# Kernel optimization log

Measured on AMD Instinct MI355X. Metric: run time of the kernel, lower is better.

Reference implementation:

```python
import jax, jax.numpy as jnp
import numpy as np

N_ROUTES = 7      # len(ROUTES): 3 unimodal + 3 bimodal + 1 trimodal routes
PC_DIM = 512      # primary capsule pose dim
MC_DIM = 128      # output (decision) capsule pose dim
K = 25            # num_classes (phenotypes)
NUM_ROUTING = 3   # routing iterations
B = 4096


def _layer_norm(x, gamma, beta, eps=1e-5):
    mu = jnp.mean(x, axis=-1, keepdims=True)
    var = jnp.var(x, axis=-1, keepdims=True)
    return (x - mu) * jax.lax.rsqrt(var + eps) * gamma + beta


def setup_inputs() -> dict:
    key = jax.random.key(0)
    ks = jax.random.split(key, 4)
    w_std = float(np.sqrt(K / (PC_DIM * N_ROUTES)))  # CapsuleFC weight init scale
    return {
        "prim_pose": jax.random.normal(ks[0], (B, N_ROUTES, PC_DIM), dtype=jnp.float32),
        "prim_act": jax.random.uniform(ks[1], (B, N_ROUTES), dtype=jnp.float32),
        "w": w_std * jax.random.normal(ks[2], (N_ROUTES, PC_DIM, K, MC_DIM), dtype=jnp.float32),
        "ln_gamma": jnp.ones((MC_DIM,), dtype=jnp.float32),
        "ln_beta": jnp.zeros((MC_DIM,), dtype=jnp.float32),
        "embedding": 0.02 * jax.random.normal(ks[3], (K, MC_DIM), dtype=jnp.float32),
        "bias": jnp.zeros((K,), dtype=jnp.float32),
    }


def reference(prim_pose, prim_act, w, ln_gamma, ln_beta, embedding, bias):
    # prim_pose: [B, N, D_in]; prim_act: [B, N]
    act = prim_act[..., None]                      # [B, N, 1]
    scale = 1.0 / np.sqrt(MC_DIM)
    # Votes are constant across routing iterations; hoist out of the loop.
    vote = jnp.einsum('bnd,ndmv->bnmv', prim_pose, w)  # [B, N, K, Dv]
    next_pose = None
    routing_coef = None
    for it in range(NUM_ROUTING):
        if next_pose is None:
            # iteration 0: uniform routing coefficients (softmax of zeros over out capsules)
            routing_coef = jnp.full((prim_pose.shape[0], N_ROUTES, K), 1.0 / K,
                                    dtype=prim_pose.dtype)
        else:
            # inverted dot-product attention: agreement between votes and current decision pose
            agree = jnp.einsum('bnmv,bmv->bnm', vote, next_pose) * scale
            routing_coef = jax.nn.softmax(agree, axis=-1)
        c = routing_coef * act                     # weight routing by primary activations
        next_pose = _layer_norm(jnp.einsum('bnm,bnmv->bmv', c, vote), ln_gamma, ln_beta)
        # act_type='ONES' -> decision activations are all ones (no effect on routing)
    logits = jnp.einsum('bmd,md->bm', next_pose, embedding) + bias  # [B, K]
    return logits, prim_act, routing_coef
```

## Files before the change

kernel.cpp:

```cpp
#include <hip/hip_runtime.h>
#include <hip/hip_bf16.h>
#include <math.h>

#define N_ROUTES 7
#define PC_DIM   512
#define MC_DIM   128
#define KCLS     25
#define BATCH    4096

#define ROW_IN   (N_ROUTES * PC_DIM)
#define JDIM     (KCLS * MC_DIM)
#define VOTE_B   (N_ROUTES * JDIM)

typedef __attribute__((ext_vector_type(8))) _Float16 half8;
typedef __attribute__((ext_vector_type(4))) float f32x4;

__device__ inline ushort f2h(float f) {
    _Float16 h = (_Float16)f;
    return __builtin_bit_cast(ushort, h);
}

__device__ inline float2 h2f2(uint u) {
    union { uint x; _Float16 h[2]; } c; c.x = u;
    return make_float2((float)c.h[0], (float)c.h[1]);
}

__device__ inline void load_lds16(const void* g, void* l) {
    __builtin_amdgcn_global_load_lds(
        (const __attribute__((address_space(1))) void*)g,
        (__attribute__((address_space(3))) void*)l, 16, 0, 0);
}

__global__ __launch_bounds__(256) void conv_pose(const float* __restrict__ p,
                                                 ushort* __restrict__ pb, int n8) {
    int i = blockIdx.x * 256 + threadIdx.x;
    if (i >= n8) return;
    const float4* s = (const float4*)p + (size_t)i * 2;
    float4 a = s[0], b = s[1];
    ushort t[8];
    t[0]=f2h(a.x); t[1]=f2h(a.y); t[2]=f2h(a.z); t[3]=f2h(a.w);
    t[4]=f2h(b.x); t[5]=f2h(b.y); t[6]=f2h(b.z); t[7]=f2h(b.w);
    *(uint4*)(pb + (size_t)i * 8) = *(uint4*)t;
}

__global__ __launch_bounds__(256) void conv_w(const float* __restrict__ w,
                                              ushort* __restrict__ wt) {
    __shared__ float t[32][65];
    const int j0 = blockIdx.x * 32, d0 = blockIdx.y * 64, r = blockIdx.z;
    const int jc = threadIdx.x & 31, dr0 = threadIdx.x >> 5;
    const float* wp = w + (size_t)r * PC_DIM * JDIM;
#pragma unroll
    for (int i = 0; i < 8; i++)
        t[jc][dr0 + i * 8] = wp[(size_t)(d0 + dr0 + i * 8) * JDIM + j0 + jc];
    __syncthreads();
    const int jr = threadIdx.x >> 3, dc = (threadIdx.x & 7) * 8;
    ushort o[8];
#pragma unroll
    for (int k = 0; k < 8; k++) o[k] = f2h(t[jr][dc + k]);
    ushort* op = wt + (size_t)r * JDIM * PC_DIM;
    *(uint4*)(op + (size_t)(j0 + jr) * PC_DIM + d0 + dc) = *(uint4*)o;
}


#define BAR() do { __builtin_amdgcn_sched_barrier(0); \
                   __builtin_amdgcn_s_barrier(); \
                   __builtin_amdgcn_sched_barrier(0); } while (0)
#define WAIT_LGKM0() do { asm volatile("s_waitcnt lgkmcnt(0)" ::: "memory"); \
                          __builtin_amdgcn_sched_barrier(0); } while (0)
#define WAIT_VM(n) do { asm volatile("s_waitcnt vmcnt(" #n ")" ::: "memory"); } while (0)

__global__ __launch_bounds__(256, 3) void vote_gemm_mfma(
        const ushort* __restrict__ poseb,
        const ushort* __restrict__ wt,
        ushort* __restrict__ vote,
        int rows) {
    __shared__ __align__(16) char smem[49152];

    int route, rowTile, jTile;
    {
        const int blk = blockIdx.x;
        if (gridDim.x == 5600) {
            const int x = blk & 7;
            const int g = blk >> 3;
            const int q = g / 25;
            jTile = g - q * 25;
            const int p = x * 28 + q;
            route = p >> 5;
            rowTile = p & 31;
        } else {
            rowTile = blk / 175;
            const int rem = blk - rowTile * 175;
            route = rem / 25;
            jTile = rem - route * 25;
        }
    }
    const int b0 = rowTile * 128;
    const int j0 = jTile * 128;

    const int tid = threadIdx.x;
    const int l = tid & 63, w = tid >> 6;
    const int wm = w >> 1, wn = w & 1;
    const int lm = l & 15, q4 = l >> 4;
    const int xr = (l >> 1) & 3;

    const ushort* Aptr = poseb + (size_t)route * PC_DIM;
    const ushort* Bptr = wt + (size_t)route * JDIM * PC_DIM;

    uint aof0, aof1, bof0, bof1;
    {
        int f, row, c, qg, ga;
        f = tid;        row = f >> 2; c = f & 3; qg = c ^ ((row >> 1) & 3);
        ga = b0 + row; if (ga >= rows) ga = rows - 1;
        aof0 = (uint)ga * ROW_IN + qg * 8;
        bof0 = (uint)(j0 + row) * PC_DIM + qg * 8;
        f = tid + 256;  row = f >> 2; c = f & 3; qg = c ^ ((row >> 1) & 3);
        ga = b0 + row; if (ga >= rows) ga = rows - 1;
        aof1 = (uint)ga * ROW_IN + qg * 8;
        bof1 = (uint)(j0 + row) * PC_DIM + qg * 8;
    }

    const int aBase = ((wm * 64 + lm) * 4 + (q4 ^ xr)) * 16;
    const int bBase = 8192 + ((wn * 64 + lm) * 4 + (q4 ^ xr)) * 16;

    f32x4 acc[4][4] = {};

#define STAGE(kt) do { \
        char* d_ = smem + (((kt) % 3) * 16384); \
        load_lds16(Aptr + aof0 + (kt) * 32, d_ + (size_t)tid * 16); \
        load_lds16(Aptr + aof1 + (kt) * 32, d_ + (size_t)(tid + 256) * 16); \
        load_lds16(Bptr + bof0 + (kt) * 32, d_ + 8192 + (size_t)tid * 16); \
        load_lds16(Bptr + bof1 + (kt) * 32, d_ + 8192 + (size_t)(tid + 256) * 16); \
    } while (0)

    STAGE(0); STAGE(1);
    WAIT_VM(4);
    BAR();

    half8 af[4], bf[4];

#pragma unroll
    for (int t = 0; t < 16; ++t) {
        if (t < 14) STAGE(t + 2);
        const char* bp_ = smem + ((t % 3) * 16384);
#pragma unroll
        for (int nt = 0; nt < 4; nt++)
            bf[nt] = *(const half8*)(bp_ + bBase + nt * 1024);
#pragma unroll
        for (int mt = 0; mt < 4; mt++)
            af[mt] = *(const half8*)(bp_ + aBase + mt * 1024);
        WAIT_LGKM0();
        __builtin_amdgcn_s_setprio(1);
#pragma unroll
        for (int mt = 0; mt < 4; mt++)
#pragma unroll
            for (int nt = 0; nt < 4; nt++)
                acc[mt][nt] = __builtin_amdgcn_mfma_f32_16x16x32_f16(
                    af[mt], bf[nt], acc[mt][nt], 0, 0, 0);
        __builtin_amdgcn_s_setprio(0);
        if (t < 14)       WAIT_VM(4);
        else if (t == 14) WAIT_VM(0);
        BAR();
    }

    float* ep = (float*)smem + w * 1088;
    const int erow = l >> 2, ec0 = (l & 3) * 16;
#pragma unroll
    for (int mt = 0; mt < 4; mt++) {
#pragma unroll
        for (int nt = 0; nt < 4; nt++)
#pragma unroll
            for (int i = 0; i < 4; i++)
                ep[(q4 * 4 + i) * 68 + nt * 16 + lm] = acc[mt][nt][i];
        asm volatile("s_waitcnt lgkmcnt(0)" ::: "memory");
        const int grow = b0 + wm * 64 + mt * 16 + erow;
        if (grow < rows) {
            ushort t16[16];
#pragma unroll
            for (int t8 = 0; t8 < 4; t8++) {
                float4 v = *(float4*)&ep[erow * 68 + ec0 + t8 * 4];
                t16[t8*4+0]=f2h(v.x); t16[t8*4+1]=f2h(v.y);
                t16[t8*4+2]=f2h(v.z); t16[t8*4+3]=f2h(v.w);
            }
            ushort* dst = vote + (size_t)grow * VOTE_B + route * JDIM + j0 + wn * 64 + ec0;
            ((uint4*)dst)[0] = ((uint4*)t16)[0];
            ((uint4*)dst)[1] = ((uint4*)t16)[1];
        }
        asm volatile("s_waitcnt lgkmcnt(0)" ::: "memory");
    }
}

__global__ __launch_bounds__(448) void routing_kernel(
        const ushort* __restrict__ vote16,
        const float* __restrict__ act,
        const float* __restrict__ gamma,
        const float* __restrict__ beta,
        const float* __restrict__ emb,
        const float* __restrict__ bias,
        float* __restrict__ out_logits,
        float* __restrict__ out_act,
        float* __restrict__ out_coef) {
    const int b = blockIdx.x;
    __shared__ float coef_s[N_ROUTES * KCLS];
    __shared__ float act_s[8];

    const int tid = threadIdx.x, l = tid & 63, wv = tid >> 6;
    const int sub = l & 15, mg = l >> 4;
    const int m = wv + 7 * mg;
    const bool mv = (m < KCLS);

    if (tid < N_ROUTES) {
        float a = act[(size_t)b * N_ROUTES + tid];
        act_s[tid] = a;
        out_act[(size_t)b * N_ROUTES + tid] = a;
    }

    float vf[N_ROUTES][8];
    if (mv) {
        const uint4* vb = (const uint4*)(vote16 + (size_t)b * VOTE_B);
#pragma unroll
        for (int n = 0; n < N_ROUTES; n++) {
            uint4 q = vb[n * 400 + m * 16 + sub];
            float2 f0 = h2f2(q.x), f1 = h2f2(q.y), f2 = h2f2(q.z), f3 = h2f2(q.w);
            vf[n][0] = f0.x; vf[n][1] = f0.y; vf[n][2] = f1.x; vf[n][3] = f1.y;
            vf[n][4] = f2.x; vf[n][5] = f2.y; vf[n][6] = f3.x; vf[n][7] = f3.y;
        }
    } else {
#pragma unroll
        for (int n = 0; n < N_ROUTES; n++)
#pragma unroll
            for (int j = 0; j < 8; j++) vf[n][j] = 0.f;
    }
    const int mc = mv ? m : 24;

    float g[8], be[8];
    *(float4*)(g)      = *(const float4*)(gamma + 8 * sub);
    *(float4*)(g + 4)  = *(const float4*)(gamma + 8 * sub + 4);
    *(float4*)(be)     = *(const float4*)(beta  + 8 * sub);
    *(float4*)(be + 4) = *(const float4*)(beta  + 8 * sub + 4);
    __syncthreads();

    const float scale = 0.088388347648318447f;
    float pose[8];

    auto update = [&](bool first) {
        float r[8];
#pragma unroll
        for (int j = 0; j < 8; j++) r[j] = 0.f;
#pragma unroll
        for (int n = 0; n < N_ROUTES; n++) {
            float c = first ? (act_s[n] * 0.04f) : (coef_s[n * KCLS + mc] * act_s[n]);
#pragma unroll
            for (int j = 0; j < 8; j++) r[j] += c * vf[n][j];
        }
        float S = 0.f, Q = 0.f;
#pragma unroll
        for (int j = 0; j < 8; j++) { S += r[j]; Q += r[j] * r[j]; }
#pragma unroll
        for (int o = 8; o; o >>= 1) {
            S += __shfl_xor(S, o);
            Q += __shfl_xor(Q, o);
        }
        float mean = S * 0.0078125f;
        float var  = Q * 0.0078125f - mean * mean;
        float rs   = rsqrtf(var + 1e-5f);
#pragma unroll
        for (int j = 0; j < 8; j++) pose[j] = (r[j] - mean) * rs * g[j] + be[j];
    };

    update(true);
    __syncthreads();

    const int sgrp = tid >> 5, slane = tid & 31;

    for (int it = 1; it < 3; it++) {
        float d[N_ROUTES];
#pragma unroll
        for (int n = 0; n < N_ROUTES; n++) {
            float t = 0.f;
#pragma unroll
            for (int j = 0; j < 8; j++) t += vf[n][j] * pose[j];
            d[n] = t;
        }
#pragma unroll
        for (int o = 8; o; o >>= 1)
#pragma unroll
            for (int n = 0; n < N_ROUTES; n++) d[n] += __shfl_xor(d[n], o);
        if (sub == 0 && mv) {
#pragma unroll
            for (int n = 0; n < N_ROUTES; n++) coef_s[n * KCLS + m] = d[n] * scale;
        }
        __syncthreads();
        if (sgrp < N_ROUTES) {
            float c = (slane < KCLS) ? coef_s[sgrp * KCLS + slane] : -1e30f;
            float mx = c;
#pragma unroll
            for (int o = 16; o; o >>= 1) mx = fmaxf(mx, __shfl_xor(mx, o, 32));
            float e = (slane < KCLS) ? expf(c - mx) : 0.f;
            float s = e;
#pragma unroll
            for (int o = 16; o; o >>= 1) s += __shfl_xor(s, o, 32);
            if (slane < KCLS) coef_s[sgrp * KCLS + slane] = e / s;
        }
        __syncthreads();
        update(false);
        if (it == 1) __syncthreads();
    }

    float e[8];
    *(float4*)(e)     = *(const float4*)(emb + mc * MC_DIM + 8 * sub);
    *(float4*)(e + 4) = *(const float4*)(emb + mc * MC_DIM + 8 * sub + 4);
    float dd = 0.f;
#pragma unroll
    for (int j = 0; j < 8; j++) dd += pose[j] * e[j];
#pragma unroll
    for (int o = 8; o; o >>= 1) dd += __shfl_xor(dd, o);
    if (sub == 0 && mv) out_logits[(size_t)b * KCLS + m] = dd + bias[m];

    if (tid < N_ROUTES * KCLS)
        out_coef[(size_t)b * (N_ROUTES * KCLS) + tid] = coef_s[tid];
}

extern "C" void kernel_launch(void* const* d_in, const int* in_sizes, int n_in,
                              void* d_out, int out_size, void* d_ws, size_t ws_size,
                              hipStream_t stream) {
    const float* pose  = (const float*)d_in[0];
    const float* act   = (const float*)d_in[1];
    const float* w     = (const float*)d_in[2];
    const float* gamma = (const float*)d_in[3];
    const float* beta  = (const float*)d_in[4];
    const float* emb   = (const float*)d_in[5];
    const float* bias  = (const float*)d_in[6];

    float* out        = (float*)d_out;
    float* out_logits = out;
    float* out_act    = out + BATCH * KCLS;
    float* out_coef   = out + BATCH * KCLS + BATCH * N_ROUTES;

    const size_t wt_bytes    = (size_t)N_ROUTES * JDIM * PC_DIM * 2;
    const size_t poseb_bytes = (size_t)BATCH * ROW_IN * 2;
    ushort* wt    = (ushort*)d_ws;
    ushort* poseb = (ushort*)((char*)d_ws + wt_bytes);
    ushort* voteh = (ushort*)((char*)d_ws + wt_bytes + poseb_bytes);

    size_t rem = ws_size > wt_bytes + poseb_bytes ? ws_size - wt_bytes - poseb_bytes : 0;
    size_t cap = rem / ((size_t)VOTE_B * 2);
    int chunk;
    if (cap >= (size_t)BATCH)  chunk = BATCH;
    else if (cap >= 128)       chunk = (int)(cap & ~(size_t)127);
    else                       chunk = (int)(cap > 0 ? cap : 1);

    conv_w<<<dim3(JDIM / 32, PC_DIM / 64, N_ROUTES), 256, 0, stream>>>(w, wt);
    const int n8 = BATCH * ROW_IN / 8;
    conv_pose<<<(n8 + 255) / 256, 256, 0, stream>>>(pose, poseb, n8);

    for (int b0 = 0; b0 < BATCH; b0 += chunk) {
        int rows = BATCH - b0 < chunk ? BATCH - b0 : chunk;
        int nRowTiles = (rows + 127) / 128;
        vote_gemm_mfma<<<nRowTiles * 175, 256, 0, stream>>>(
            poseb + (size_t)b0 * ROW_IN, wt, voteh, rows);
        routing_kernel<<<rows, 448, 0, stream>>>(
            voteh,
            act + (size_t)b0 * N_ROUTES,
            gamma, beta, emb, bias,
            out_logits + (size_t)b0 * KCLS,
            out_act    + (size_t)b0 * N_ROUTES,
            out_coef   + (size_t)b0 * N_ROUTES * KCLS);
    }
}
```

Before: 335.5 us.

## Double-buffer LDS fragment reads in vote GEMM to overlap with MFMA

Restructures the vote GEMM main loop so fragments for the next k-tile are read from LDS into a second register set while MFMAs run on the current set. This removes the explicit lgkmcnt(0) wait before each MFMA block. The epilogue now alternates between two LDS staging regions so the trailing lgkmcnt wait can be dropped. The extra fragment registers raise register pressure, which may hurt occupancy at three blocks per CU.

```diff
diff --git a/kernel.cpp b/kernel.cpp
--- a/kernel.cpp
+++ b/kernel.cpp
@@ -65,8 +65,6 @@
 #define BAR() do { __builtin_amdgcn_sched_barrier(0); \
                    __builtin_amdgcn_s_barrier(); \
                    __builtin_amdgcn_sched_barrier(0); } while (0)
-#define WAIT_LGKM0() do { asm volatile("s_waitcnt lgkmcnt(0)" ::: "memory"); \
-                          __builtin_amdgcn_sched_barrier(0); } while (0)
 #define WAIT_VM(n) do { asm volatile("s_waitcnt vmcnt(" #n ")" ::: "memory"); } while (0)
 
 __global__ __launch_bounds__(256, 3) void vote_gemm_mfma(
@@ -132,40 +130,53 @@
         load_lds16(Bptr + bof1 + (kt) * 32, d_ + 8192 + (size_t)(tid + 256) * 16); \
     } while (0)
 
+#define READF(kt, AF, BF) do { \
+        const char* rp_ = smem + (((kt) % 3) * 16384); \
+        _Pragma("unroll") for (int i_ = 0; i_ < 4; i_++) { \
+            AF[i_] = *(const half8*)(rp_ + aBase + i_ * 1024); \
+            BF[i_] = *(const half8*)(rp_ + bBase + i_ * 1024); \
+        } \
+    } while (0)
+
+#define MFMA16(AF, BF) do { \
+        _Pragma("unroll") for (int mt_ = 0; mt_ < 4; mt_++) \
+        _Pragma("unroll") for (int nt_ = 0; nt_ < 4; nt_++) \
+            acc[mt_][nt_] = __builtin_amdgcn_mfma_f32_16x16x32_f16( \
+                AF[mt_], BF[nt_], acc[mt_][nt_], 0, 0, 0); \
+    } while (0)
+
     STAGE(0); STAGE(1);
     WAIT_VM(4);
     BAR();
-
-    half8 af[4], bf[4];
-
-#pragma unroll
-    for (int t = 0; t < 16; ++t) {
-        if (t < 14) STAGE(t + 2);
-        const char* bp_ = smem + ((t % 3) * 16384);
-#pragma unroll
-        for (int nt = 0; nt < 4; nt++)
-            bf[nt] = *(const half8*)(bp_ + bBase + nt * 1024);
-#pragma unroll
-        for (int mt = 0; mt < 4; mt++)
-            af[mt] = *(const half8*)(bp_ + aBase + mt * 1024);
-        WAIT_LGKM0();
-        __builtin_amdgcn_s_setprio(1);
-#pragma unroll
-        for (int mt = 0; mt < 4; mt++)
-#pragma unroll
-            for (int nt = 0; nt < 4; nt++)
-                acc[mt][nt] = __builtin_amdgcn_mfma_f32_16x16x32_f16(
-                    af[mt], bf[nt], acc[mt][nt], 0, 0, 0);
-        __builtin_amdgcn_s_setprio(0);
-        if (t < 14)       WAIT_VM(4);
-        else if (t == 14) WAIT_VM(0);
+    half8 ax[4], bx[4], ay[4], by[4];
+    READF(0, ax, bx);
+    STAGE(2);
+
+#pragma unroll
+    for (int tt = 0; tt < 7; ++tt) {
+        const int t = 2 * tt;
+        WAIT_VM(4);
         BAR();
-    }
-
-    float* ep = (float*)smem + w * 1088;
+        READF(t + 1, ay, by);
+        STAGE(t + 3);
+        MFMA16(ax, bx);
+        WAIT_VM(4);
+        BAR();
+        READF(t + 2, ax, bx);
+        if (t + 4 <= 15) STAGE(t + 4);
+        MFMA16(ay, by);
+    }
+    WAIT_VM(0);
+    BAR();
+    READF(15, ay, by);
+    MFMA16(ax, bx);
+    MFMA16(ay, by);
+    BAR();
+
     const int erow = l >> 2, ec0 = (l & 3) * 16;
 #pragma unroll
     for (int mt = 0; mt < 4; mt++) {
+        float* ep = (float*)smem + w * 1088 + (mt & 1) * 4352;
 #pragma unroll
         for (int nt = 0; nt < 4; nt++)
 #pragma unroll
@@ -185,7 +196,6 @@
             ((uint4*)dst)[0] = ((uint4*)t16)[0];
             ((uint4*)dst)[1] = ((uint4*)t16)[1];
         }
-        asm volatile("s_waitcnt lgkmcnt(0)" ::: "memory");
     }
 }
 
```

Result: no change. 333.1 us (-0.7%).
